# Kernel tuning notes

Measured on AMD Instinct MI355X. Metric: run time of the kernel, lower is better.

## Reference

```python
import jax, jax.numpy as jnp
import numpy as np
from jax import lax

DIM = 512; NUM_HEADS = 8; WS = 2; POOL = 3
HEAD_DIM = DIM // NUM_HEADS
L_HEADS = int(NUM_HEADS * 0.5); L_DIM = L_HEADS * HEAD_DIM
H_HEADS = NUM_HEADS - L_HEADS; H_DIM = H_HEADS * HEAD_DIM
SCALE = HEAD_DIM ** (-0.5)


def setup_inputs():
    key = jax.random.key(0)
    ks = jax.random.split(key, 8)
    B, Hh, Ww = 8, 64, 64
    N = Hh * Ww
    s = lambda fan: 1.0 / np.sqrt(fan)
    return {
        'x': jax.random.normal(ks[0], (B, N, DIM), jnp.float32),
        'H': Hh,
        'l_q_w': jax.random.normal(ks[1], (DIM, L_DIM), jnp.float32) * s(DIM),
        'l_kv_w': jax.random.normal(ks[2], (DIM, 2 * L_DIM), jnp.float32) * s(DIM),
        'l_proj_w': jax.random.normal(ks[3], (L_DIM, L_DIM), jnp.float32) * s(L_DIM),
        'l_proj_b': jax.random.normal(ks[4], (L_DIM,), jnp.float32) * 0.01,
        'h_qkv_w': jax.random.normal(ks[5], (DIM, H_DIM), jnp.float32) * s(DIM),
        'h_proj_w': jax.random.normal(ks[6], (H_DIM, H_DIM), jnp.float32) * s(H_DIM),
        'h_proj_b': jax.random.normal(ks[7], (H_DIM,), jnp.float32) * 0.01,
    }


def _avgpool3_same(x):
    # x: [M, ws, ws, C]; 3x3 avg pool, stride 1, pad 1, count_include_pad=False
    ssum = lax.reduce_window(x, jnp.float32(0.0), lax.add,
                             (1, POOL, POOL, 1), (1, 1, 1, 1),
                             ((0, 0), (1, 1), (1, 1), (0, 0)))
    ones = jnp.ones(x.shape[1:3], x.dtype)
    cnt = lax.reduce_window(ones, jnp.float32(0.0), lax.add,
                            (POOL, POOL), (1, 1), ((1, 1), (1, 1)))
    return ssum / cnt[None, :, :, None]


def _hifi(x, h_qkv_w, h_proj_w, h_proj_b):
    B, H, W, C = x.shape
    hg, wg = H // WS, W // WS
    x = x @ h_qkv_w  # [B,H,W,H_DIM]
    # partition into ws x ws windows: [B*hg*wg, ws, ws, H_DIM]
    xw = x.reshape(B, hg, WS, wg, WS, H_DIM).transpose(0, 1, 3, 2, 4, 5)
    xw = xw.reshape(B * hg * wg, WS, WS, H_DIM)
    xw = _avgpool3_same(xw) - xw
    xw = xw.reshape(B, hg, wg, WS, WS, H_DIM).transpose(0, 1, 3, 2, 4, 5)
    xw = xw.reshape(B, H, W, H_DIM)
    return xw @ h_proj_w + h_proj_b


def _lofi(x, l_q_w, l_kv_w, l_proj_w, l_proj_b):
    B, H, W, C = x.shape
    q = (x @ l_q_w).reshape(B, H * W, L_HEADS, HEAD_DIM).transpose(0, 2, 1, 3)
    # spatial reduction: avg pool ws stride ws -> [B, H/ws * W/ws, C]
    xp = x.reshape(B, H // WS, WS, W // WS, WS, C).mean(axis=(2, 4))
    xp = xp.reshape(B, -1, C)
    kv = (xp @ l_kv_w).reshape(B, -1, 2, L_HEADS, HEAD_DIM)
    k = kv[:, :, 0].transpose(0, 2, 1, 3)  # [B,h,M,d]
    v = kv[:, :, 1].transpose(0, 2, 1, 3)
    attn = jax.nn.softmax(jnp.einsum('bhnd,bhmd->bhnm', q, k) * SCALE, axis=-1)
    out = jnp.einsum('bhnm,bhmd->bhnd', attn, v)
    out = out.transpose(0, 2, 1, 3).reshape(B, H, W, L_DIM)
    return out @ l_proj_w + l_proj_b


def reference(x, H, l_q_w, l_kv_w, l_proj_w, l_proj_b, h_qkv_w, h_proj_w, h_proj_b):
    B, N, C = x.shape
    W = N // H
    xg = x.reshape(B, H, W, C)
    hi = _hifi(xg, h_qkv_w, h_proj_w, h_proj_b)
    lo = _lofi(xg, l_q_w, l_kv_w, l_proj_w, l_proj_b)
    out = jnp.concatenate([hi, lo], axis=-1)  # [B,H,W,C]
    return out.reshape(B, N, C)
```

## Files before the change

### kernel.cpp

```cpp
#include <hip/hip_runtime.h>

typedef __bf16 bf16x8 __attribute__((ext_vector_type(8)));
typedef float  f32x4  __attribute__((ext_vector_type(4)));
typedef unsigned int u32x4 __attribute__((ext_vector_type(4)));
typedef unsigned short u16x8 __attribute__((ext_vector_type(8)));
typedef unsigned short u16x4 __attribute__((ext_vector_type(4)));

__device__ __forceinline__ unsigned short f2bf(float f) {
    return __builtin_bit_cast(unsigned short, (__bf16)f);
}
__device__ __forceinline__ float bf2f(unsigned short s) {
    return (float)__builtin_bit_cast(__bf16, s);
}
__device__ __forceinline__ bf16x8 as_bf16x8(u32x4 v) {
    return __builtin_bit_cast(bf16x8, v);
}

#define AS1 __attribute__((address_space(1)))
#define AS3 __attribute__((address_space(3)))
__device__ __forceinline__ void gload_lds16(const void* g, void* l) {
    __builtin_amdgcn_global_load_lds((const AS1 void*)g, (AS3 void*)l, 16, 0, 0);
}


__global__ __launch_bounds__(256) void k_cast_x(const float* __restrict__ x,
                                                unsigned short* __restrict__ xb) {
    int i = blockIdx.x * 256 + threadIdx.x;
    f32x4 v = ((const f32x4*)x)[i];
    u16x4 o = { f2bf(v[0]), f2bf(v[1]), f2bf(v[2]), f2bf(v[3]) };
    ((u16x4*)xb)[i] = o;
}

__global__ __launch_bounds__(256) void k_pool(const unsigned short* __restrict__ xb,
                                              unsigned short* __restrict__ xpb) {
    int t = blockIdx.x * 256 + threadIdx.x;
    int r = t >> 6, c8 = (t & 63) << 3;
    int b = r >> 10, hw = r & 1023;
    int h2 = hw >> 5, w2 = hw & 31;
    int n00 = (h2 << 7) + (w2 << 1);
    const unsigned short* base = xb + ((size_t)(b << 12) + n00) * 512 + c8;
    u16x8 v0 = *(const u16x8*)base;
    u16x8 v1 = *(const u16x8*)(base + 512);
    u16x8 v2 = *(const u16x8*)(base + 64 * 512);
    u16x8 v3 = *(const u16x8*)(base + 65 * 512);
    u16x8 o;
#pragma unroll
    for (int j = 0; j < 8; j++)
        o[j] = f2bf(0.25f * (bf2f(v0[j]) + bf2f(v1[j]) + bf2f(v2[j]) + bf2f(v3[j])));
    *(u16x8*)(xpb + (size_t)r * 512 + c8) = o;
}

__global__ __launch_bounds__(256) void k_weights(
        const float* __restrict__ h_qkv_w, const float* __restrict__ l_q_w,
        const float* __restrict__ l_kv_w, const float* __restrict__ h_proj_w,
        const float* __restrict__ l_proj_w,
        unsigned short* __restrict__ wcatT, unsigned short* __restrict__ lkvT,
        unsigned short* __restrict__ hprojT, unsigned short* __restrict__ lprojT) {
    int i = blockIdx.x * 256 + threadIdx.x;
    if (i < 262144) {
        int n = i >> 9, k = i & 511;
        float v = (n < 256) ? h_qkv_w[k * 256 + n] : l_q_w[k * 256 + (n - 256)];
        wcatT[i] = f2bf(v);
    } else if (i < 524288) {
        int j = i - 262144; int n = j >> 9, k = j & 511;
        lkvT[j] = f2bf(l_kv_w[k * 512 + n]);
    } else if (i < 589824) {
        int j = i - 524288; int n = j >> 8, k = j & 255;
        hprojT[j] = f2bf(h_proj_w[k * 256 + n]);
    } else {
        int j = i - 589824; int n = j >> 8, k = j & 255;
        lprojT[j] = f2bf(l_proj_w[k * 256 + n]);
    }
}

__global__ __launch_bounds__(256) void k_vt(const unsigned short* __restrict__ kvm,
                                            unsigned short* __restrict__ vT) {
    int t = blockIdx.x * 256 + threadIdx.x;
    int bh = t >> 13;
    int rem = t & 8191;
    int ck = rem >> 6;
    int d = rem & 63;
    int b = bh >> 2, h = bh & 3;
    const unsigned short* src = kvm + ((size_t)(b * 1024 + ck * 8)) * 512 + 256 + h * 64 + d;
    u16x8 v;
#pragma unroll
    for (int j = 0; j < 8; j++) v[j] = src[j * 512];
    *(u16x8*)(vT + ((size_t)(bh * 64 + d)) * 1024 + ck * 8) = v;
}

__global__ __launch_bounds__(256) void k_hifi(const unsigned short* __restrict__ hqq,
                                              unsigned short* __restrict__ dbuf) {
    int t = blockIdx.x * 256 + threadIdx.x;
    int win = t >> 5, c8 = (t & 31) << 3;
    int b = win >> 10, wi = win & 1023;
    int h2 = wi >> 5, w2 = wi & 31;
    int n00 = (b << 12) + (h2 << 7) + (w2 << 1);
    const unsigned short* p = hqq + (size_t)n00 * 512 + c8;
    u16x8 a0 = *(const u16x8*)p;
    u16x8 a1 = *(const u16x8*)(p + 512);
    u16x8 a2 = *(const u16x8*)(p + 64 * 512);
    u16x8 a3 = *(const u16x8*)(p + 65 * 512);
    u16x8 o0, o1, o2, o3;
#pragma unroll
    for (int j = 0; j < 8; j++) {
        float f0 = bf2f(a0[j]), f1 = bf2f(a1[j]), f2 = bf2f(a2[j]), f3 = bf2f(a3[j]);
        float m = 0.25f * (f0 + f1 + f2 + f3);
        o0[j] = f2bf(m - f0); o1[j] = f2bf(m - f1);
        o2[j] = f2bf(m - f2); o3[j] = f2bf(m - f3);
    }
    unsigned short* q = dbuf + (size_t)n00 * 256 + c8;
    *(u16x8*)q = o0;
    *(u16x8*)(q + 256) = o1;
    *(u16x8*)(q + 64 * 256) = o2;
    *(u16x8*)(q + 65 * 256) = o3;
}

__global__ __launch_bounds__(256, 2) void k_gemm(
        const unsigned short* __restrict__ A,
        const unsigned short* __restrict__ Bt,
        unsigned short* __restrict__ Cb,
        float* __restrict__ Cf,
        const float* __restrict__ bias,
        int K, int ldc, int coloff) {
    __shared__ __align__(16) unsigned short As[128 * 32];
    __shared__ __align__(16) unsigned short Bs[128 * 32];
    const int tid = threadIdx.x;
    const int wave = tid >> 6, lane = tid & 63;
    const int m16 = lane & 15, quad = lane >> 4;
    const int wr = wave >> 1, wc = wave & 1;
    const size_t row0 = (size_t)blockIdx.x * 128;
    const int col0 = blockIdx.y * 128;

    const int srow = lane >> 2;
    const int scol = (lane & 3) * 8;
    const unsigned short* Ap0 = A + (row0 + wave * 32 + srow) * (size_t)K + scol;
    const unsigned short* Ap1 = Ap0 + (size_t)16 * K;
    const unsigned short* Bp0 = Bt + (size_t)(col0 + wave * 32 + srow) * K + scol;
    const unsigned short* Bp1 = Bp0 + (size_t)16 * K;
    unsigned short* Al0 = As + wave * 1024;
    unsigned short* Al1 = As + wave * 1024 + 512;
    unsigned short* Bl0 = Bs + wave * 1024;
    unsigned short* Bl1 = Bs + wave * 1024 + 512;

    f32x4 acc[4][4] = {};

    for (int k0 = 0; k0 < K; k0 += 32) {
        __syncthreads();
        gload_lds16(Ap0 + k0, Al0);
        gload_lds16(Ap1 + k0, Al1);
        gload_lds16(Bp0 + k0, Bl0);
        gload_lds16(Bp1 + k0, Bl1);
        __syncthreads();
        bf16x8 af[4], bfr[4];
#pragma unroll
        for (int mi = 0; mi < 4; mi++)
            af[mi] = as_bf16x8(*(const u32x4*)(As + (wr * 64 + mi * 16 + m16) * 32 + quad * 8));
#pragma unroll
        for (int ni = 0; ni < 4; ni++)
            bfr[ni] = as_bf16x8(*(const u32x4*)(Bs + (wc * 64 + ni * 16 + m16) * 32 + quad * 8));
#pragma unroll
        for (int mi = 0; mi < 4; mi++)
#pragma unroll
            for (int ni = 0; ni < 4; ni++)
                acc[mi][ni] = __builtin_amdgcn_mfma_f32_16x16x32_bf16(af[mi], bfr[ni], acc[mi][ni], 0, 0, 0);
    }

#pragma unroll
    for (int mi = 0; mi < 4; mi++) {
#pragma unroll
        for (int ni = 0; ni < 4; ni++) {
            const int colL = col0 + wc * 64 + ni * 16 + m16;
            const float bv = bias ? bias[colL] : 0.0f;
#pragma unroll
            for (int r = 0; r < 4; r++) {
                const size_t row = row0 + wr * 64 + mi * 16 + quad * 4 + r;
                float v = acc[mi][ni][r] + bv;
                if (Cf) Cf[row * ldc + coloff + colL] = v;
                else    Cb[row * ldc + coloff + colL] = f2bf(v);
            }
        }
    }
}

__global__ __launch_bounds__(256, 2) void k_attn(
        const unsigned short* __restrict__ hqq,
        const unsigned short* __restrict__ kvm,
        const unsigned short* __restrict__ vT,
        unsigned short* __restrict__ aout) {
    __shared__ __align__(16) unsigned short Kb[2][64 * 72];
    __shared__ __align__(16) unsigned short Vb[2][64 * 72];
    __shared__ __align__(16) unsigned short Pl[4][32 * 74];
    const int tid = threadIdx.x;
    const int wave = tid >> 6, lane = tid & 63;
    const int m16 = lane & 15, quad = lane >> 4;
    const int qtile = blockIdx.x, bh = blockIdx.y;
    const int b = bh >> 2, h = bh & 3;

    bf16x8 qf[2][2];
    const size_t qrow0 = (size_t)b * 4096 + qtile * 128 + wave * 32;
#pragma unroll
    for (int qh = 0; qh < 2; qh++) {
        const unsigned short* qp = hqq + (qrow0 + qh * 16 + m16) * 512 + 256 + h * 64 + quad * 8;
        qf[qh][0] = as_bf16x8(*(const u32x4*)qp);
        qf[qh][1] = as_bf16x8(*(const u32x4*)(qp + 32));
    }

    f32x4 o[2][4] = {};
    f32x4 lp[2] = {};

    const int sr = tid >> 3;
    const int sc = tid & 7;
    const unsigned short* kg = kvm + ((size_t)b * 1024) * 512 + h * 64 + sc * 8;
    const unsigned short* vg = vT + ((size_t)bh * 64) * 1024 + sc * 8;

    u32x4 stg[4];
    stg[0] = *(const u32x4*)(kg + (size_t)sr * 512);
    stg[1] = *(const u32x4*)(kg + (size_t)(sr + 32) * 512);
    stg[2] = *(const u32x4*)(vg + (size_t)sr * 1024);
    stg[3] = *(const u32x4*)(vg + (size_t)(sr + 32) * 1024);
    *(u32x4*)&Kb[0][sr * 72 + sc * 8] = stg[0];
    *(u32x4*)&Kb[0][(sr + 32) * 72 + sc * 8] = stg[1];
    *(u32x4*)&Vb[0][sr * 72 + sc * 8] = stg[2];
    *(u32x4*)&Vb[0][(sr + 32) * 72 + sc * 8] = stg[3];

    for (int it = 0; it < 16; ++it) {
        const int cur = it & 1, nxt = cur ^ 1;
        __syncthreads();
        if (it + 1 < 16) {
            const size_t kvb = (size_t)(it + 1) * 64;
            stg[0] = *(const u32x4*)(kg + (kvb + sr) * 512);
            stg[1] = *(const u32x4*)(kg + (kvb + sr + 32) * 512);
            stg[2] = *(const u32x4*)(vg + kvb + (size_t)sr * 1024);
            stg[3] = *(const u32x4*)(vg + kvb + (size_t)(sr + 32) * 1024);
        }

        bf16x8 kf[4][2];
#pragma unroll
        for (int nt = 0; nt < 4; nt++) {
            const unsigned short* kp = &Kb[cur][(nt * 16 + m16) * 72 + quad * 8];
            kf[nt][0] = as_bf16x8(*(const u32x4*)kp);
            kf[nt][1] = as_bf16x8(*(const u32x4*)(kp + 32));
        }
        f32x4 s[2][4] = {};
#pragma unroll
        for (int qh = 0; qh < 2; qh++)
#pragma unroll
            for (int nt = 0; nt < 4; nt++) {
                s[qh][nt] = __builtin_amdgcn_mfma_f32_16x16x32_bf16(qf[qh][0], kf[nt][0], s[qh][nt], 0, 0, 0);
                s[qh][nt] = __builtin_amdgcn_mfma_f32_16x16x32_bf16(qf[qh][1], kf[nt][1], s[qh][nt], 0, 0, 0);
            }

#pragma unroll
        for (int qh = 0; qh < 2; qh++)
#pragma unroll
            for (int nt = 0; nt < 4; nt++)
#pragma unroll
                for (int r = 0; r < 4; r++) {
                    float pv = __expf(s[qh][nt][r] * 0.125f);
                    lp[qh][r] += pv;
                    Pl[wave][(qh * 16 + quad * 4 + r) * 74 + nt * 16 + m16] = f2bf(pv);
                }
        asm volatile("s_waitcnt lgkmcnt(0)" ::: "memory");

        bf16x8 vf[4][2];
#pragma unroll
        for (int nt = 0; nt < 4; nt++) {
            const unsigned short* vp = &Vb[cur][(nt * 16 + m16) * 72 + quad * 8];
            vf[nt][0] = as_bf16x8(*(const u32x4*)vp);
            vf[nt][1] = as_bf16x8(*(const u32x4*)(vp + 32));
        }
#pragma unroll
        for (int qh = 0; qh < 2; qh++) {
            const bf16x8 pf0 = as_bf16x8(*(const u32x4*)&Pl[wave][(qh * 16 + m16) * 74 + quad * 8]);
            const bf16x8 pf1 = as_bf16x8(*(const u32x4*)&Pl[wave][(qh * 16 + m16) * 74 + 32 + quad * 8]);
#pragma unroll
            for (int nt = 0; nt < 4; nt++) {
                o[qh][nt] = __builtin_amdgcn_mfma_f32_16x16x32_bf16(pf0, vf[nt][0], o[qh][nt], 0, 0, 0);
                o[qh][nt] = __builtin_amdgcn_mfma_f32_16x16x32_bf16(pf1, vf[nt][1], o[qh][nt], 0, 0, 0);
            }
        }

        if (it + 1 < 16) {
            *(u32x4*)&Kb[nxt][sr * 72 + sc * 8] = stg[0];
            *(u32x4*)&Kb[nxt][(sr + 32) * 72 + sc * 8] = stg[1];
            *(u32x4*)&Vb[nxt][sr * 72 + sc * 8] = stg[2];
            *(u32x4*)&Vb[nxt][(sr + 32) * 72 + sc * 8] = stg[3];
        }
    }

#pragma unroll
    for (int qh = 0; qh < 2; qh++) {
        f32x4 linv;
#pragma unroll
        for (int r = 0; r < 4; r++) {
            float l = lp[qh][r];
            l += __shfl_xor(l, 1);
            l += __shfl_xor(l, 2);
            l += __shfl_xor(l, 4);
            l += __shfl_xor(l, 8);
            linv[r] = __builtin_amdgcn_rcpf(l);
        }
#pragma unroll
        for (int nt = 0; nt < 4; nt++)
#pragma unroll
            for (int r = 0; r < 4; r++)
                aout[(qrow0 + qh * 16 + quad * 4 + r) * 256 + h * 64 + nt * 16 + m16] =
                    f2bf(o[qh][nt][r] * linv[r]);
    }
}


extern "C" void kernel_launch(void* const* d_in, const int* in_sizes, int n_in,
                              void* d_out, int out_size, void* d_ws, size_t ws_size,
                              hipStream_t stream) {
    (void)in_sizes; (void)n_in; (void)out_size; (void)ws_size;
    const float* x        = (const float*)d_in[0];
    const float* l_q_w    = (const float*)d_in[2];
    const float* l_kv_w   = (const float*)d_in[3];
    const float* l_proj_w = (const float*)d_in[4];
    const float* l_proj_b = (const float*)d_in[5];
    const float* h_qkv_w  = (const float*)d_in[6];
    const float* h_proj_w = (const float*)d_in[7];
    const float* h_proj_b = (const float*)d_in[8];
    float* out = (float*)d_out;

    char* ws = (char*)d_ws;
    unsigned short* xb     = (unsigned short*)(ws);
    unsigned short* dbuf   = (unsigned short*)(ws);
    unsigned short* aout   = (unsigned short*)(ws + 16777216);
    unsigned short* xpb    = (unsigned short*)(ws + 33554432);
    unsigned short* vTbuf  = (unsigned short*)(ws + 33554432);
    unsigned short* wcatT  = (unsigned short*)(ws + 41943040);
    unsigned short* lkvT   = (unsigned short*)(ws + 42467328);
    unsigned short* hprojT = (unsigned short*)(ws + 42991616);
    unsigned short* lprojT = (unsigned short*)(ws + 43122688);
    unsigned short* hqq    = (unsigned short*)(ws + 43253760);
    unsigned short* kvm    = (unsigned short*)(ws + 76808192);

    k_cast_x <<<16384, 256, 0, stream>>>(x, xb);
    k_pool   <<<2048,  256, 0, stream>>>(xb, xpb);
    k_weights<<<2560,  256, 0, stream>>>(h_qkv_w, l_q_w, l_kv_w, h_proj_w, l_proj_w,
                                         wcatT, lkvT, hprojT, lprojT);
    k_gemm<<<dim3(256, 4), 256, 0, stream>>>(xb, wcatT, hqq, nullptr, nullptr, 512, 512, 0);
    k_gemm<<<dim3(64, 4), 256, 0, stream>>>(xpb, lkvT, kvm, nullptr, nullptr, 512, 512, 0);
    k_vt<<<1024, 256, 0, stream>>>(kvm, vTbuf);
    k_hifi<<<1024, 256, 0, stream>>>(hqq, dbuf);
    k_gemm<<<dim3(256, 2), 256, 0, stream>>>(dbuf, hprojT, nullptr, out, h_proj_b, 256, 512, 0);
    k_attn<<<dim3(32, 32), 256, 0, stream>>>(hqq, kvm, vTbuf, aout);
    k_gemm<<<dim3(256, 2), 256, 0, stream>>>(aout, lprojT, nullptr, out, l_proj_b, 256, 512, 256);
}
```

Measured before the change: 281.2 us.

## Restructure attention kernel: 8 waves per block, transposed S MFMA, packed P stores

The attention kernel now runs 512 threads (8 waves) per block, each block covering 256 query rows, so every K/V tile staged in LDS is shared by twice as many waves and each thread stages only one K and one V vector per tile. QK^T is computed as K·Q (transposed) so each lane holds four consecutive key scores for one query, which lets the P tile be written to LDS as packed 4-element stores and reduces the row-sum to a per-lane scalar. The final normalisation uses cross-quad shuffles plus a broadcast shuffle in place of the 16-lane reduction tree. The changes increase LDS usage per block and registers are constrained by the 512-thread launch bounds, which may affect occupancy.

```diff
diff --git a/kernel.cpp b/kernel.cpp
--- a/kernel.cpp
+++ b/kernel.cpp
@@ -182,14 +182,14 @@
     }
 }
 
-__global__ __launch_bounds__(256, 2) void k_attn(
+__global__ __launch_bounds__(512, 4) void k_attn(
         const unsigned short* __restrict__ hqq,
         const unsigned short* __restrict__ kvm,
         const unsigned short* __restrict__ vT,
         unsigned short* __restrict__ aout) {
     __shared__ __align__(16) unsigned short Kb[2][64 * 72];
     __shared__ __align__(16) unsigned short Vb[2][64 * 72];
-    __shared__ __align__(16) unsigned short Pl[4][32 * 74];
+    __shared__ __align__(16) unsigned short Pl[8][32 * 72];
     const int tid = threadIdx.x;
     const int wave = tid >> 6, lane = tid & 63;
     const int m16 = lane & 15, quad = lane >> 4;
@@ -197,7 +197,7 @@
     const int b = bh >> 2, h = bh & 3;
 
     bf16x8 qf[2][2];
-    const size_t qrow0 = (size_t)b * 4096 + qtile * 128 + wave * 32;
+    const size_t qrow0 = (size_t)b * 4096 + qtile * 256 + wave * 32;
 #pragma unroll
     for (int qh = 0; qh < 2; qh++) {
         const unsigned short* qp = hqq + (qrow0 + qh * 16 + m16) * 512 + 256 + h * 64 + quad * 8;
@@ -206,100 +206,85 @@
     }
 
     f32x4 o[2][4] = {};
-    f32x4 lp[2] = {};
+    float lp[2] = {0.f, 0.f};
 
     const int sr = tid >> 3;
     const int sc = tid & 7;
     const unsigned short* kg = kvm + ((size_t)b * 1024) * 512 + h * 64 + sc * 8;
     const unsigned short* vg = vT + ((size_t)bh * 64) * 1024 + sc * 8;
 
-    u32x4 stg[4];
-    stg[0] = *(const u32x4*)(kg + (size_t)sr * 512);
-    stg[1] = *(const u32x4*)(kg + (size_t)(sr + 32) * 512);
-    stg[2] = *(const u32x4*)(vg + (size_t)sr * 1024);
-    stg[3] = *(const u32x4*)(vg + (size_t)(sr + 32) * 1024);
-    *(u32x4*)&Kb[0][sr * 72 + sc * 8] = stg[0];
-    *(u32x4*)&Kb[0][(sr + 32) * 72 + sc * 8] = stg[1];
-    *(u32x4*)&Vb[0][sr * 72 + sc * 8] = stg[2];
-    *(u32x4*)&Vb[0][(sr + 32) * 72 + sc * 8] = stg[3];
+    u32x4 stg0 = *(const u32x4*)(kg + (size_t)sr * 512);
+    u32x4 stg1 = *(const u32x4*)(vg + (size_t)sr * 1024);
+    *(u32x4*)&Kb[0][sr * 72 + sc * 8] = stg0;
+    *(u32x4*)&Vb[0][sr * 72 + sc * 8] = stg1;
 
     for (int it = 0; it < 16; ++it) {
         const int cur = it & 1, nxt = cur ^ 1;
         __syncthreads();
         if (it + 1 < 16) {
             const size_t kvb = (size_t)(it + 1) * 64;
-            stg[0] = *(const u32x4*)(kg + (kvb + sr) * 512);
-            stg[1] = *(const u32x4*)(kg + (kvb + sr + 32) * 512);
-            stg[2] = *(const u32x4*)(vg + kvb + (size_t)sr * 1024);
-            stg[3] = *(const u32x4*)(vg + kvb + (size_t)(sr + 32) * 1024);
-        }
-
-        bf16x8 kf[4][2];
-#pragma unroll
-        for (int nt = 0; nt < 4; nt++) {
-            const unsigned short* kp = &Kb[cur][(nt * 16 + m16) * 72 + quad * 8];
-            kf[nt][0] = as_bf16x8(*(const u32x4*)kp);
-            kf[nt][1] = as_bf16x8(*(const u32x4*)(kp + 32));
-        }
-        f32x4 s[2][4] = {};
-#pragma unroll
-        for (int qh = 0; qh < 2; qh++)
-#pragma unroll
-            for (int nt = 0; nt < 4; nt++) {
-                s[qh][nt] = __builtin_amdgcn_mfma_f32_16x16x32_bf16(qf[qh][0], kf[nt][0], s[qh][nt], 0, 0, 0);
-                s[qh][nt] = __builtin_amdgcn_mfma_f32_16x16x32_bf16(qf[qh][1], kf[nt][1], s[qh][nt], 0, 0, 0);
+            stg0 = *(const u32x4*)(kg + (kvb + sr) * 512);
+            stg1 = *(const u32x4*)(vg + kvb + (size_t)sr * 1024);
+        }
+
+#pragma unroll
+        for (int mt = 0; mt < 4; mt++) {
+            const unsigned short* kp = &Kb[cur][(mt * 16 + m16) * 72 + quad * 8];
+            const bf16x8 kf0 = as_bf16x8(*(const u32x4*)kp);
+            const bf16x8 kf1 = as_bf16x8(*(const u32x4*)(kp + 32));
+            f32x4 st[2] = {};
+#pragma unroll
+            for (int qh = 0; qh < 2; qh++) {
+                st[qh] = __builtin_amdgcn_mfma_f32_16x16x32_bf16(kf0, qf[qh][0], st[qh], 0, 0, 0);
+                st[qh] = __builtin_amdgcn_mfma_f32_16x16x32_bf16(kf1, qf[qh][1], st[qh], 0, 0, 0);
             }
-
-#pragma unroll
-        for (int qh = 0; qh < 2; qh++)
-#pragma unroll
-            for (int nt = 0; nt < 4; nt++)
-#pragma unroll
-                for (int r = 0; r < 4; r++) {
-                    float pv = __expf(s[qh][nt][r] * 0.125f);
-                    lp[qh][r] += pv;
-                    Pl[wave][(qh * 16 + quad * 4 + r) * 74 + nt * 16 + m16] = f2bf(pv);
-                }
+#pragma unroll
+            for (int qh = 0; qh < 2; qh++) {
+                float p0 = __expf(st[qh][0] * 0.125f);
+                float p1 = __expf(st[qh][1] * 0.125f);
+                float p2 = __expf(st[qh][2] * 0.125f);
+                float p3 = __expf(st[qh][3] * 0.125f);
+                lp[qh] += (p0 + p1) + (p2 + p3);
+                u16x4 pk = { f2bf(p0), f2bf(p1), f2bf(p2), f2bf(p3) };
+                *(u16x4*)&Pl[wave][(qh * 16 + m16) * 72 + mt * 16 + quad * 4] = pk;
+            }
+        }
         asm volatile("s_waitcnt lgkmcnt(0)" ::: "memory");
 
-        bf16x8 vf[4][2];
+        bf16x8 pf[2][2];
+#pragma unroll
+        for (int qh = 0; qh < 2; qh++) {
+            const unsigned short* pp = &Pl[wave][(qh * 16 + m16) * 72 + quad * 8];
+            pf[qh][0] = as_bf16x8(*(const u32x4*)pp);
+            pf[qh][1] = as_bf16x8(*(const u32x4*)(pp + 32));
+        }
 #pragma unroll
         for (int nt = 0; nt < 4; nt++) {
             const unsigned short* vp = &Vb[cur][(nt * 16 + m16) * 72 + quad * 8];
-            vf[nt][0] = as_bf16x8(*(const u32x4*)vp);
-            vf[nt][1] = as_bf16x8(*(const u32x4*)(vp + 32));
-        }
-#pragma unroll
-        for (int qh = 0; qh < 2; qh++) {
-            const bf16x8 pf0 = as_bf16x8(*(const u32x4*)&Pl[wave][(qh * 16 + m16) * 74 + quad * 8]);
-            const bf16x8 pf1 = as_bf16x8(*(const u32x4*)&Pl[wave][(qh * 16 + m16) * 74 + 32 + quad * 8]);
-#pragma unroll
-            for (int nt = 0; nt < 4; nt++) {
-                o[qh][nt] = __builtin_amdgcn_mfma_f32_16x16x32_bf16(pf0, vf[nt][0], o[qh][nt], 0, 0, 0);
-                o[qh][nt] = __builtin_amdgcn_mfma_f32_16x16x32_bf16(pf1, vf[nt][1], o[qh][nt], 0, 0, 0);
+            const bf16x8 vf0 = as_bf16x8(*(const u32x4*)vp);
+            const bf16x8 vf1 = as_bf16x8(*(const u32x4*)(vp + 32));
+#pragma unroll
+            for (int qh = 0; qh < 2; qh++) {
+                o[qh][nt] = __builtin_amdgcn_mfma_f32_16x16x32_bf16(pf[qh][0], vf0, o[qh][nt], 0, 0, 0);
+                o[qh][nt] = __builtin_amdgcn_mfma_f32_16x16x32_bf16(pf[qh][1], vf1, o[qh][nt], 0, 0, 0);
             }
         }
 
         if (it + 1 < 16) {
-            *(u32x4*)&Kb[nxt][sr * 72 + sc * 8] = stg[0];
-            *(u32x4*)&Kb[nxt][(sr + 32) * 72 + sc * 8] = stg[1];
-            *(u32x4*)&Vb[nxt][sr * 72 + sc * 8] = stg[2];
-            *(u32x4*)&Vb[nxt][(sr + 32) * 72 + sc * 8] = stg[3];
+            *(u32x4*)&Kb[nxt][sr * 72 + sc * 8] = stg0;
+            *(u32x4*)&Vb[nxt][sr * 72 + sc * 8] = stg1;
         }
     }
 
 #pragma unroll
     for (int qh = 0; qh < 2; qh++) {
+        float l = lp[qh];
+        l += __shfl_xor(l, 16);
+        l += __shfl_xor(l, 32);
         f32x4 linv;
 #pragma unroll
-        for (int r = 0; r < 4; r++) {
-            float l = lp[qh][r];
-            l += __shfl_xor(l, 1);
-            l += __shfl_xor(l, 2);
-            l += __shfl_xor(l, 4);
-            l += __shfl_xor(l, 8);
-            linv[r] = __builtin_amdgcn_rcpf(l);
-        }
+        for (int r = 0; r < 4; r++)
+            linv[r] = __builtin_amdgcn_rcpf(__shfl(l, quad * 4 + r));
 #pragma unroll
         for (int nt = 0; nt < 4; nt++)
 #pragma unroll
@@ -346,6 +331,6 @@
     k_vt<<<1024, 256, 0, stream>>>(kvm, vTbuf);
     k_hifi<<<1024, 256, 0, stream>>>(hqq, dbuf);
     k_gemm<<<dim3(256, 2), 256, 0, stream>>>(dbuf, hprojT, nullptr, out, h_proj_b, 256, 512, 0);
-    k_attn<<<dim3(32, 32), 256, 0, stream>>>(hqq, kvm, vTbuf, aout);
+    k_attn<<<dim3(16, 32), 512, 0, stream>>>(hqq, kvm, vTbuf, aout);
     k_gemm<<<dim3(256, 2), 256, 0, stream>>>(aout, lprojT, nullptr, out, l_proj_b, 256, 512, 256);
 }
```

After: 265.4 us. 1.06x faster.
